# Optimization experiments

Measured on AMD Instinct MI355X. Metric: run time of the kernel, lower is better.

The kernel has to match this reference:

```python
import math
import jax, jax.numpy as jnp
import numpy as np

N_HEAD = 16

def setup_inputs() -> dict:
    key = jax.random.key(0)
    k1, k2, k3 = jax.random.split(key, 3)
    B, T, C = 4, 2048, 1024
    x = jax.random.normal(k1, (B, T, C), dtype=jnp.float32)
    Wqkv = jax.random.normal(k2, (C, 3 * C), dtype=jnp.float32) * (1.0 / math.sqrt(C))
    bqkv = jnp.zeros((3 * C,), dtype=jnp.float32)
    Wproj = jax.random.normal(k3, (C, C), dtype=jnp.float32) * (1.0 / math.sqrt(C))
    bproj = jnp.zeros((C,), dtype=jnp.float32)
    return {"x": x, "Wqkv": Wqkv, "bqkv": bqkv, "Wproj": Wproj, "bproj": bproj}

def reference(x, Wqkv, bqkv, Wproj, bproj):
    B, T, C = x.shape
    H = N_HEAD
    D = C // H
    # fused QKV projection
    qkv = x @ Wqkv + bqkv                      # [B,T,3C]
    qkv = qkv.reshape(B, T, 3, H, D).transpose(0, 2, 3, 1, 4)  # [B,3,H,T,D]
    q, k, v = qkv[:, 0], qkv[:, 1], qkv[:, 2]  # each [B,H,T,D]
    scale = 1.0 / math.sqrt(D)
    att = jnp.einsum('bhtd,bhsd->bhts', q, k) * scale  # [B,H,T,T]
    # causal mask: disallow s > t
    mask = jnp.triu(jnp.ones((T, T), dtype=bool), k=1)
    att = jnp.where(mask, jnp.float32(-1e9), att)
    att = jax.nn.softmax(att, axis=-1)
    y = jnp.einsum('bhts,bhsd->bhtd', att, v)  # [B,H,T,D]
    y = y.transpose(0, 2, 1, 3).reshape(B, T, C)
    y = y @ Wproj + bproj
    return y
```

## Files before the change

### kernel.cpp

```cpp
#include <hip/hip_runtime.h>
#include <hip/hip_bf16.h>

#define B_ 4
#define T_ 2048
#define C_ 1024
#define H_ 16
#define D_ 64

typedef __attribute__((ext_vector_type(8))) short short8;
typedef __attribute__((ext_vector_type(4))) float f32x4;

#define QSCALE 0.18033688011112042f

static __device__ __forceinline__ unsigned short f2bf(float f) {
  unsigned u = __float_as_uint(f);
  u += 0x7fff + ((u >> 16) & 1);
  return (unsigned short)(u >> 16);
}

static __device__ __forceinline__ float fast_exp2(float x) {
#if __has_builtin(__builtin_amdgcn_exp2f)
  return __builtin_amdgcn_exp2f(x);
#else
  return exp2f(x);
#endif
}

#define GL2LDS16(g, l)                                              \
  __builtin_amdgcn_global_load_lds(                                 \
      (const __attribute__((address_space(1))) void*)(g),           \
      (__attribute__((address_space(3))) void*)(l), 16, 0, 0)

__global__ __launch_bounds__(256) void convert_bf16(const float* __restrict__ in,
                                                    ushort* __restrict__ out) {
  const size_t i = ((size_t)blockIdx.x * 256 + threadIdx.x) * 4;
  float4 v = *(const float4*)(in + i);
  ushort4 o = {f2bf(v.x), f2bf(v.y), f2bf(v.z), f2bf(v.w)};
  *(ushort4*)(out + i) = o;
}

__global__ __launch_bounds__(256) void convert_transpose(
    const float* __restrict__ in, ushort* __restrict__ out, int K, int N) {
  __shared__ ushort tile[32][33];
  const int k0 = blockIdx.y << 5, n0 = blockIdx.x << 5;
  const int r = threadIdx.x >> 3;
  const int c4 = (threadIdx.x & 7) << 2;
  float4 v = *(const float4*)(in + (size_t)(k0 + r) * N + n0 + c4);
  tile[c4 + 0][r] = f2bf(v.x);
  tile[c4 + 1][r] = f2bf(v.y);
  tile[c4 + 2][r] = f2bf(v.z);
  tile[c4 + 3][r] = f2bf(v.w);
  __syncthreads();
  ushort4 o = {tile[r][c4], tile[r][c4 + 1], tile[r][c4 + 2], tile[r][c4 + 3]};
  *(ushort4*)(out + (size_t)(n0 + r) * K + k0 + c4) = o;
}

__global__ __launch_bounds__(256) void gemm_qkv_mfma(
    const ushort* __restrict__ A,
    const ushort* __restrict__ Bt,
    const float* __restrict__ bias,
    ushort* __restrict__ q, ushort* __restrict__ k, ushort* __restrict__ v) {
  __shared__ __align__(16) ushort As[128 * 32];
  __shared__ __align__(16) ushort Bs[128 * 32];
  const int tid = threadIdx.x;
  const int wave = tid >> 6, lane = tid & 63;
  const int c = lane & 15, quad = lane >> 4;
  const int wm = wave & 1, wn = wave >> 1;
  const int m0 = blockIdx.y << 7;
  const int n0 = blockIdx.x << 7;

  f32x4 acc[4][4];
#pragma unroll
  for (int i = 0; i < 4; ++i)
#pragma unroll
    for (int j = 0; j < 4; ++j) acc[i][j] = (f32x4){0.f, 0.f, 0.f, 0.f};

  for (int k0 = 0; k0 < C_; k0 += 32) {
    __syncthreads();
#pragma unroll
    for (int p = 0; p < 2; ++p) {
      const int flat = p * 4096 + wave * 1024 + lane * 16;
      const int row = flat >> 6, ke = (flat & 63) >> 1;
      GL2LDS16(A + (size_t)(m0 + row) * C_ + k0 + ke,
               (char*)As + p * 4096 + wave * 1024);
      GL2LDS16(Bt + (size_t)(n0 + row) * C_ + k0 + ke,
               (char*)Bs + p * 4096 + wave * 1024);
    }
    __syncthreads();

    short8 af[4], bf[4];
#pragma unroll
    for (int i = 0; i < 4; ++i)
      af[i] = *(const short8*)(As + (wm * 64 + i * 16 + c) * 32 + quad * 8);
#pragma unroll
    for (int j = 0; j < 4; ++j)
      bf[j] = *(const short8*)(Bs + (wn * 64 + j * 16 + c) * 32 + quad * 8);
#pragma unroll
    for (int i = 0; i < 4; ++i)
#pragma unroll
      for (int j = 0; j < 4; ++j)
        acc[i][j] =
            __builtin_amdgcn_mfma_f32_16x16x32_bf16(af[i], bf[j], acc[i][j], 0, 0, 0);
  }

  const int s = n0 >> 10;
  if (s == 2) {
#pragma unroll
    for (int j = 0; j < 4; ++j) {
      const int n = n0 + wn * 64 + j * 16 + c;
      const int h = (n >> 6) & 15, d = n & 63;
      const float bval = bias[n];
#pragma unroll
      for (int i = 0; i < 4; ++i) {
        const int m = m0 + wm * 64 + i * 16 + quad * 4;
        const int b = m >> 11, t = m & 2047;
        ushort4 pk = {f2bf(acc[i][j][0] + bval), f2bf(acc[i][j][1] + bval),
                      f2bf(acc[i][j][2] + bval), f2bf(acc[i][j][3] + bval)};
        *(ushort4*)(v + (((size_t)((b << 4) + h) << 6) + d) * T_ + t) = pk;
      }
    }
  } else {
    ushort* outp = (s == 0) ? q : k;
    const float sc = (s == 0) ? QSCALE : 1.0f;
#pragma unroll
    for (int j = 0; j < 4; ++j) {
      const int n = n0 + wn * 64 + j * 16 + c;
      const int h = (n >> 6) & 15, d = n & 63;
      const float bval = bias[n];
#pragma unroll
      for (int i = 0; i < 4; ++i) {
#pragma unroll
        for (int r = 0; r < 4; ++r) {
          const int m = m0 + wm * 64 + i * 16 + quad * 4 + r;
          const int b = m >> 11, t = m & 2047;
          outp[(((size_t)((b << 4) + h) << 11) + t) * 64 + d] =
              f2bf((acc[i][j][r] + bval) * sc);
        }
      }
    }
  }
}

__global__ __launch_bounds__(256) void gemm_proj_mfma(
    const ushort* __restrict__ A,
    const ushort* __restrict__ Bt,
    const float* __restrict__ bias,
    float* __restrict__ out) {
  __shared__ __align__(16) ushort As[128 * 32];
  __shared__ __align__(16) ushort Bs[128 * 32];
  const int tid = threadIdx.x;
  const int wave = tid >> 6, lane = tid & 63;
  const int c = lane & 15, quad = lane >> 4;
  const int wm = wave & 1, wn = wave >> 1;
  const int m0 = blockIdx.y << 7;
  const int n0 = blockIdx.x << 7;

  f32x4 acc[4][4];
#pragma unroll
  for (int i = 0; i < 4; ++i)
#pragma unroll
    for (int j = 0; j < 4; ++j) acc[i][j] = (f32x4){0.f, 0.f, 0.f, 0.f};

  for (int k0 = 0; k0 < C_; k0 += 32) {
    __syncthreads();
#pragma unroll
    for (int p = 0; p < 2; ++p) {
      const int flat = p * 4096 + wave * 1024 + lane * 16;
      const int row = flat >> 6, ke = (flat & 63) >> 1;
      GL2LDS16(A + (size_t)(m0 + row) * C_ + k0 + ke,
               (char*)As + p * 4096 + wave * 1024);
      GL2LDS16(Bt + (size_t)(n0 + row) * C_ + k0 + ke,
               (char*)Bs + p * 4096 + wave * 1024);
    }
    __syncthreads();

    short8 af[4], bf[4];
#pragma unroll
    for (int i = 0; i < 4; ++i)
      af[i] = *(const short8*)(As + (wm * 64 + i * 16 + c) * 32 + quad * 8);
#pragma unroll
    for (int j = 0; j < 4; ++j)
      bf[j] = *(const short8*)(Bs + (wn * 64 + j * 16 + c) * 32 + quad * 8);
#pragma unroll
    for (int i = 0; i < 4; ++i)
#pragma unroll
      for (int j = 0; j < 4; ++j)
        acc[i][j] =
            __builtin_amdgcn_mfma_f32_16x16x32_bf16(af[i], bf[j], acc[i][j], 0, 0, 0);
  }

#pragma unroll
  for (int j = 0; j < 4; ++j) {
    const int n = n0 + wn * 64 + j * 16 + c;
    const float bval = bias[n];
#pragma unroll
    for (int i = 0; i < 4; ++i) {
#pragma unroll
      for (int r = 0; r < 4; ++r) {
        const int m = m0 + wm * 64 + i * 16 + quad * 4 + r;
        out[(size_t)m * C_ + n] = acc[i][j][r] + bval;
      }
    }
  }
}

__global__ __launch_bounds__(256) void attn(const ushort* __restrict__ q,
                                            const ushort* __restrict__ k,
                                            const ushort* __restrict__ v,
                                            ushort* __restrict__ y2) {
  const int qt = 31 - (int)(blockIdx.x >> 6);
  const int bh = blockIdx.x & 63;
  const int t0 = qt << 6;
  const int w = threadIdx.x >> 6;
  const int lane = threadIdx.x & 63;
  const int c = lane & 15;
  const int quad = lane >> 4;

  const ushort* qp = q + (size_t)bh * T_ * D_;
  const ushort* kp = k + (size_t)bh * T_ * D_;
  const ushort* vp = v + (size_t)bh * D_ * T_;

  __shared__ __align__(16) ushort Ks[64][72];
  __shared__ __align__(16) ushort Vs[64][72];
  __shared__ __align__(16) ushort Ps[4][16][72];

  short8 qf0, qf1;
  {
    const ushort* qrow = qp + (size_t)(t0 + 16 * w + c) * D_;
    qf0 = *(const short8*)(qrow + quad * 8);
    qf1 = *(const short8*)(qrow + 32 + quad * 8);
  }

  const int srow = threadIdx.x >> 2;
  const int soff = (threadIdx.x & 3) << 4;

  uint4 ka, kb, va, vb;
  {
    const ushort* ks = kp + (size_t)srow * D_ + soff;
    const ushort* vs = vp + (size_t)srow * T_ + soff;
    ka = *(const uint4*)(ks);
    kb = *(const uint4*)(ks + 8);
    va = *(const uint4*)(vs);
    vb = *(const uint4*)(vs + 8);
  }

  f32x4 o[4];
  float l_i[4];
#pragma unroll
  for (int nt = 0; nt < 4; ++nt) o[nt] = (f32x4){0.f, 0.f, 0.f, 0.f};
#pragma unroll
  for (int r = 0; r < 4; ++r) l_i[r] = 0.f;

  for (int ib = 0; ib <= qt; ++ib) {
    __syncthreads();
    *(uint4*)(&Ks[srow][soff]) = ka;
    *(uint4*)(&Ks[srow][soff + 8]) = kb;
    *(uint4*)(&Vs[srow][soff]) = va;
    *(uint4*)(&Vs[srow][soff + 8]) = vb;
    __syncthreads();

    if (ib < qt) {
      const int s1 = (ib + 1) << 6;
      const ushort* ks = kp + (size_t)(s1 + srow) * D_ + soff;
      const ushort* vs = vp + (size_t)srow * T_ + s1 + soff;
      ka = *(const uint4*)(ks);
      kb = *(const uint4*)(ks + 8);
      va = *(const uint4*)(vs);
      vb = *(const uint4*)(vs + 8);
    }

    f32x4 s[4];
#pragma unroll
    for (int nt = 0; nt < 4; ++nt) {
      short8 kf0 = *(const short8*)(&Ks[nt * 16 + c][quad * 8]);
      short8 kf1 = *(const short8*)(&Ks[nt * 16 + c][32 + quad * 8]);
      f32x4 acc = (f32x4){0.f, 0.f, 0.f, 0.f};
      acc = __builtin_amdgcn_mfma_f32_16x16x32_bf16(qf0, kf0, acc, 0, 0, 0);
      acc = __builtin_amdgcn_mfma_f32_16x16x32_bf16(qf1, kf1, acc, 0, 0, 0);
      s[nt] = acc;
    }

    if (ib == qt) {
#pragma unroll
      for (int nt = 0; nt < 4; ++nt)
#pragma unroll
        for (int r = 0; r < 4; ++r)
          if (nt * 16 + c > 16 * w + 4 * quad + r) s[nt][r] = -1e30f;
    }

#pragma unroll
    for (int nt = 0; nt < 4; ++nt) {
#pragma unroll
      for (int r = 0; r < 4; ++r) {
        float p = fast_exp2(s[nt][r]);
        l_i[r] += p;
        Ps[w][4 * quad + r][nt * 16 + c] = f2bf(p);
      }
    }

    short8 pf0 = *(const short8*)(&Ps[w][c][quad * 8]);
    short8 pf1 = *(const short8*)(&Ps[w][c][32 + quad * 8]);
#pragma unroll
    for (int nt = 0; nt < 4; ++nt) {
      short8 vf0 = *(const short8*)(&Vs[nt * 16 + c][quad * 8]);
      short8 vf1 = *(const short8*)(&Vs[nt * 16 + c][32 + quad * 8]);
      o[nt] = __builtin_amdgcn_mfma_f32_16x16x32_bf16(pf0, vf0, o[nt], 0, 0, 0);
      o[nt] = __builtin_amdgcn_mfma_f32_16x16x32_bf16(pf1, vf1, o[nt], 0, 0, 0);
    }
  }

  float linv[4];
#pragma unroll
  for (int r = 0; r < 4; ++r) {
    float ls = l_i[r];
#pragma unroll
    for (int off = 1; off < 16; off <<= 1) ls += __shfl_xor(ls, off);
    linv[r] = 1.0f / ls;
  }

  const int b = bh >> 4, h = bh & 15;
#pragma unroll
  for (int nt = 0; nt < 4; ++nt)
#pragma unroll
    for (int r = 0; r < 4; ++r) {
      const int row = t0 + 16 * w + 4 * quad + r;
      y2[(size_t)(b * T_ + row) * C_ + h * D_ + nt * 16 + c] =
          f2bf(o[nt][r] * linv[r]);
    }
}

extern "C" void kernel_launch(void* const* d_in, const int* in_sizes, int n_in,
                              void* d_out, int out_size, void* d_ws,
                              size_t ws_size, hipStream_t stream) {
  const float* x = (const float*)d_in[0];
  const float* Wqkv = (const float*)d_in[1];
  const float* bqkv = (const float*)d_in[2];
  const float* Wproj = (const float*)d_in[3];
  const float* bproj = (const float*)d_in[4];
  float* out = (float*)d_out;

  const size_t per = (size_t)B_ * H_ * T_ * D_;
  ushort* q = (ushort*)d_ws;
  ushort* k = q + per;
  ushort* v = k + per;
  ushort* y2 = v + per;
  ushort* xb = y2 + per;
  ushort* Wqkvt = xb + per;
  ushort* Wprojt = Wqkvt + 3 * C_ * C_;

  convert_bf16<<<dim3(8192), 256, 0, stream>>>(x, xb);
  convert_transpose<<<dim3(96, 32), 256, 0, stream>>>(Wqkv, Wqkvt, C_, 3 * C_);
  convert_transpose<<<dim3(32, 32), 256, 0, stream>>>(Wproj, Wprojt, C_, C_);

  gemm_qkv_mfma<<<dim3(24, 64), 256, 0, stream>>>(xb, Wqkvt, bqkv, q, k, v);
  attn<<<dim3(2048), 256, 0, stream>>>(q, k, v, y2);
  gemm_proj_mfma<<<dim3(8, 64), 256, 0, stream>>>(y2, Wprojt, bproj, out);
}
```

Baseline: 268.1 us.

## Fuse prepass kernels, swizzle GEMM LDS layout, widen attention query tile

Merges the three conversion kernels into one launch. Applies an XOR swizzle to the GEMM LDS tiles so fragment reads avoid bank conflicts. Doubles the attention query tile to 128 rows per block, with each wave handling two 16-row groups, so each loaded K/V tile serves more queries. It also computes S^T so probabilities are written with vector stores. The trade-off is more registers in attention and half as many blocks.

```diff
diff --git a/kernel.cpp b/kernel.cpp
--- a/kernel.cpp
+++ b/kernel.cpp
@@ -31,18 +31,29 @@
       (const __attribute__((address_space(1))) void*)(g),           \
       (__attribute__((address_space(3))) void*)(l), 16, 0, 0)
 
-__global__ __launch_bounds__(256) void convert_bf16(const float* __restrict__ in,
-                                                    ushort* __restrict__ out) {
-  const size_t i = ((size_t)blockIdx.x * 256 + threadIdx.x) * 4;
-  float4 v = *(const float4*)(in + i);
-  ushort4 o = {f2bf(v.x), f2bf(v.y), f2bf(v.z), f2bf(v.w)};
-  *(ushort4*)(out + i) = o;
-}
-
-__global__ __launch_bounds__(256) void convert_transpose(
-    const float* __restrict__ in, ushort* __restrict__ out, int K, int N) {
+__global__ __launch_bounds__(256) void prepass(
+    const float* __restrict__ x, const float* __restrict__ Wq,
+    const float* __restrict__ Wp, ushort* __restrict__ xb,
+    ushort* __restrict__ Wqt, ushort* __restrict__ Wpt) {
   __shared__ ushort tile[32][33];
-  const int k0 = blockIdx.y << 5, n0 = blockIdx.x << 5;
+  const int bid = blockIdx.x;
+  if (bid < 8192) {
+    const size_t i = ((size_t)bid * 256 + threadIdx.x) * 4;
+    float4 vv = *(const float4*)(x + i);
+    ushort4 o = {f2bf(vv.x), f2bf(vv.y), f2bf(vv.z), f2bf(vv.w)};
+    *(ushort4*)(xb + i) = o;
+    return;
+  }
+  const float* in;
+  ushort* out;
+  int N, tix;
+  if (bid < 8192 + 3072) {
+    in = Wq; out = Wqt; N = 3 * C_; tix = bid - 8192;
+  } else {
+    in = Wp; out = Wpt; N = C_; tix = bid - 11264;
+  }
+  const int nT = N >> 5;
+  const int k0 = (tix / nT) << 5, n0 = (tix % nT) << 5;
   const int r = threadIdx.x >> 3;
   const int c4 = (threadIdx.x & 7) << 2;
   float4 v = *(const float4*)(in + (size_t)(k0 + r) * N + n0 + c4);
@@ -52,14 +63,27 @@
   tile[c4 + 3][r] = f2bf(v.w);
   __syncthreads();
   ushort4 o = {tile[r][c4], tile[r][c4 + 1], tile[r][c4 + 2], tile[r][c4 + 3]};
-  *(ushort4*)(out + (size_t)(n0 + r) * K + k0 + c4) = o;
+  *(ushort4*)(out + (size_t)(n0 + r) * C_ + k0 + c4) = o;
+}
+
+static __device__ __forceinline__ void swz_src(int wave, int lane, int p,
+                                               int& row, int& off) {
+  const int f = p * 256 + wave * 64 + lane;
+  const int P = f >> 3, pos = f & 7;
+  const int x = pos ^ (P & 7);
+  row = 2 * P + (x >> 2);
+  off = (x & 3) * 8;
+}
+static __device__ __forceinline__ int swz_frag(int r, int quad) {
+  const int P = r >> 1;
+  const int pos = (((r & 1) << 2) | quad) ^ (P & 7);
+  return (P * 8 + pos) * 16;
 }
 
 __global__ __launch_bounds__(256) void gemm_qkv_mfma(
-    const ushort* __restrict__ A,
-    const ushort* __restrict__ Bt,
-    const float* __restrict__ bias,
-    ushort* __restrict__ q, ushort* __restrict__ k, ushort* __restrict__ v) {
+    const ushort* __restrict__ A, const ushort* __restrict__ Bt,
+    const float* __restrict__ bias, ushort* __restrict__ q,
+    ushort* __restrict__ k, ushort* __restrict__ v) {
   __shared__ __align__(16) ushort As[128 * 32];
   __shared__ __align__(16) ushort Bs[128 * 32];
   const int tid = threadIdx.x;
@@ -69,6 +93,15 @@
   const int m0 = blockIdx.y << 7;
   const int n0 = blockIdx.x << 7;
 
+  int srcRow[2], srcOff[2];
+#pragma unroll
+  for (int p = 0; p < 2; ++p) swz_src(wave, lane, p, srcRow[p], srcOff[p]);
+  int fOffA[4], fOffB[4];
+#pragma unroll
+  for (int i = 0; i < 4; ++i) fOffA[i] = swz_frag(wm * 64 + i * 16 + c, quad);
+#pragma unroll
+  for (int j = 0; j < 4; ++j) fOffB[j] = swz_frag(wn * 64 + j * 16 + c, quad);
+
   f32x4 acc[4][4];
 #pragma unroll
   for (int i = 0; i < 4; ++i)
@@ -79,11 +112,9 @@
     __syncthreads();
 #pragma unroll
     for (int p = 0; p < 2; ++p) {
-      const int flat = p * 4096 + wave * 1024 + lane * 16;
-      const int row = flat >> 6, ke = (flat & 63) >> 1;
-      GL2LDS16(A + (size_t)(m0 + row) * C_ + k0 + ke,
+      GL2LDS16(A + (size_t)(m0 + srcRow[p]) * C_ + k0 + srcOff[p],
                (char*)As + p * 4096 + wave * 1024);
-      GL2LDS16(Bt + (size_t)(n0 + row) * C_ + k0 + ke,
+      GL2LDS16(Bt + (size_t)(n0 + srcRow[p]) * C_ + k0 + srcOff[p],
                (char*)Bs + p * 4096 + wave * 1024);
     }
     __syncthreads();
@@ -91,10 +122,10 @@
     short8 af[4], bf[4];
 #pragma unroll
     for (int i = 0; i < 4; ++i)
-      af[i] = *(const short8*)(As + (wm * 64 + i * 16 + c) * 32 + quad * 8);
+      af[i] = *(const short8*)((const char*)As + fOffA[i]);
 #pragma unroll
     for (int j = 0; j < 4; ++j)
-      bf[j] = *(const short8*)(Bs + (wn * 64 + j * 16 + c) * 32 + quad * 8);
+      bf[j] = *(const short8*)((const char*)Bs + fOffB[j]);
 #pragma unroll
     for (int i = 0; i < 4; ++i)
 #pragma unroll
@@ -142,10 +173,8 @@
 }
 
 __global__ __launch_bounds__(256) void gemm_proj_mfma(
-    const ushort* __restrict__ A,
-    const ushort* __restrict__ Bt,
-    const float* __restrict__ bias,
-    float* __restrict__ out) {
+    const ushort* __restrict__ A, const ushort* __restrict__ Bt,
+    const float* __restrict__ bias, float* __restrict__ out) {
   __shared__ __align__(16) ushort As[128 * 32];
   __shared__ __align__(16) ushort Bs[128 * 32];
   const int tid = threadIdx.x;
@@ -155,6 +184,15 @@
   const int m0 = blockIdx.y << 7;
   const int n0 = blockIdx.x << 7;
 
+  int srcRow[2], srcOff[2];
+#pragma unroll
+  for (int p = 0; p < 2; ++p) swz_src(wave, lane, p, srcRow[p], srcOff[p]);
+  int fOffA[4], fOffB[4];
+#pragma unroll
+  for (int i = 0; i < 4; ++i) fOffA[i] = swz_frag(wm * 64 + i * 16 + c, quad);
+#pragma unroll
+  for (int j = 0; j < 4; ++j) fOffB[j] = swz_frag(wn * 64 + j * 16 + c, quad);
+
   f32x4 acc[4][4];
 #pragma unroll
   for (int i = 0; i < 4; ++i)
@@ -165,11 +203,9 @@
     __syncthreads();
 #pragma unroll
     for (int p = 0; p < 2; ++p) {
-      const int flat = p * 4096 + wave * 1024 + lane * 16;
-      const int row = flat >> 6, ke = (flat & 63) >> 1;
-      GL2LDS16(A + (size_t)(m0 + row) * C_ + k0 + ke,
+      GL2LDS16(A + (size_t)(m0 + srcRow[p]) * C_ + k0 + srcOff[p],
                (char*)As + p * 4096 + wave * 1024);
-      GL2LDS16(Bt + (size_t)(n0 + row) * C_ + k0 + ke,
+      GL2LDS16(Bt + (size_t)(n0 + srcRow[p]) * C_ + k0 + srcOff[p],
                (char*)Bs + p * 4096 + wave * 1024);
     }
     __syncthreads();
@@ -177,10 +213,10 @@
     short8 af[4], bf[4];
 #pragma unroll
     for (int i = 0; i < 4; ++i)
-      af[i] = *(const short8*)(As + (wm * 64 + i * 16 + c) * 32 + quad * 8);
+      af[i] = *(const short8*)((const char*)As + fOffA[i]);
 #pragma unroll
     for (int j = 0; j < 4; ++j)
-      bf[j] = *(const short8*)(Bs + (wn * 64 + j * 16 + c) * 32 + quad * 8);
+      bf[j] = *(const short8*)((const char*)Bs + fOffB[j]);
 #pragma unroll
     for (int i = 0; i < 4; ++i)
 #pragma unroll
@@ -208,9 +244,9 @@
                                             const ushort* __restrict__ k,
                                             const ushort* __restrict__ v,
                                             ushort* __restrict__ y2) {
-  const int qt = 31 - (int)(blockIdx.x >> 6);
+  const int qt = 15 - (int)(blockIdx.x >> 6);
   const int bh = blockIdx.x & 63;
-  const int t0 = qt << 6;
+  const int t0 = qt << 7;
   const int w = threadIdx.x >> 6;
   const int lane = threadIdx.x & 63;
   const int c = lane & 15;
@@ -222,13 +258,14 @@
 
   __shared__ __align__(16) ushort Ks[64][72];
   __shared__ __align__(16) ushort Vs[64][72];
-  __shared__ __align__(16) ushort Ps[4][16][72];
-
-  short8 qf0, qf1;
-  {
-    const ushort* qrow = qp + (size_t)(t0 + 16 * w + c) * D_;
-    qf0 = *(const short8*)(qrow + quad * 8);
-    qf1 = *(const short8*)(qrow + 32 + quad * 8);
+  __shared__ __align__(16) ushort Ps[4][32][72];
+
+  short8 qf[2][2];
+#pragma unroll
+  for (int g = 0; g < 2; ++g) {
+    const ushort* qrow = qp + (size_t)(t0 + 32 * w + 16 * g + c) * D_;
+    qf[g][0] = *(const short8*)(qrow + quad * 8);
+    qf[g][1] = *(const short8*)(qrow + 32 + quad * 8);
   }
 
   const int srow = threadIdx.x >> 2;
@@ -244,14 +281,16 @@
     vb = *(const uint4*)(vs + 8);
   }
 
-  f32x4 o[4];
-  float l_i[4];
-#pragma unroll
-  for (int nt = 0; nt < 4; ++nt) o[nt] = (f32x4){0.f, 0.f, 0.f, 0.f};
-#pragma unroll
-  for (int r = 0; r < 4; ++r) l_i[r] = 0.f;
-
-  for (int ib = 0; ib <= qt; ++ib) {
+  f32x4 o[2][4];
+  float l_i[2] = {0.f, 0.f};
+#pragma unroll
+  for (int g = 0; g < 2; ++g)
+#pragma unroll
+    for (int dt = 0; dt < 4; ++dt) o[g][dt] = (f32x4){0.f, 0.f, 0.f, 0.f};
+
+  const int nb = 2 * qt + 2;
+  for (int ib = 0; ib < nb; ++ib) {
+    const int s0 = ib << 6;
     __syncthreads();
     *(uint4*)(&Ks[srow][soff]) = ka;
     *(uint4*)(&Ks[srow][soff + 8]) = kb;
@@ -259,7 +298,7 @@
     *(uint4*)(&Vs[srow][soff + 8]) = vb;
     __syncthreads();
 
-    if (ib < qt) {
+    if (ib + 1 < nb) {
       const int s1 = (ib + 1) << 6;
       const ushort* ks = kp + (size_t)(s1 + srow) * D_ + soff;
       const ushort* vs = vp + (size_t)srow * T_ + s1 + soff;
@@ -269,64 +308,83 @@
       vb = *(const uint4*)(vs + 8);
     }
 
-    f32x4 s[4];
-#pragma unroll
-    for (int nt = 0; nt < 4; ++nt) {
-      short8 kf0 = *(const short8*)(&Ks[nt * 16 + c][quad * 8]);
-      short8 kf1 = *(const short8*)(&Ks[nt * 16 + c][32 + quad * 8]);
-      f32x4 acc = (f32x4){0.f, 0.f, 0.f, 0.f};
-      acc = __builtin_amdgcn_mfma_f32_16x16x32_bf16(qf0, kf0, acc, 0, 0, 0);
-      acc = __builtin_amdgcn_mfma_f32_16x16x32_bf16(qf1, kf1, acc, 0, 0, 0);
-      s[nt] = acc;
-    }
-
-    if (ib == qt) {
-#pragma unroll
-      for (int nt = 0; nt < 4; ++nt)
-#pragma unroll
-        for (int r = 0; r < 4; ++r)
-          if (nt * 16 + c > 16 * w + 4 * quad + r) s[nt][r] = -1e30f;
-    }
-
-#pragma unroll
-    for (int nt = 0; nt < 4; ++nt) {
-#pragma unroll
-      for (int r = 0; r < 4; ++r) {
-        float p = fast_exp2(s[nt][r]);
-        l_i[r] += p;
-        Ps[w][4 * quad + r][nt * 16 + c] = f2bf(p);
-      }
-    }
-
-    short8 pf0 = *(const short8*)(&Ps[w][c][quad * 8]);
-    short8 pf1 = *(const short8*)(&Ps[w][c][32 + quad * 8]);
-#pragma unroll
-    for (int nt = 0; nt < 4; ++nt) {
-      short8 vf0 = *(const short8*)(&Vs[nt * 16 + c][quad * 8]);
-      short8 vf1 = *(const short8*)(&Vs[nt * 16 + c][32 + quad * 8]);
-      o[nt] = __builtin_amdgcn_mfma_f32_16x16x32_bf16(pf0, vf0, o[nt], 0, 0, 0);
-      o[nt] = __builtin_amdgcn_mfma_f32_16x16x32_bf16(pf1, vf1, o[nt], 0, 0, 0);
-    }
-  }
-
-  float linv[4];
-#pragma unroll
-  for (int r = 0; r < 4; ++r) {
-    float ls = l_i[r];
-#pragma unroll
-    for (int off = 1; off < 16; off <<= 1) ls += __shfl_xor(ls, off);
-    linv[r] = 1.0f / ls;
+#pragma unroll
+    for (int g = 0; g < 2; ++g) {
+      f32x4 st[4];
+#pragma unroll
+      for (int kt = 0; kt < 4; ++kt) {
+        short8 af0 = *(const short8*)(&Ks[kt * 16 + c][quad * 8]);
+        short8 af1 = *(const short8*)(&Ks[kt * 16 + c][32 + quad * 8]);
+        f32x4 a = (f32x4){0.f, 0.f, 0.f, 0.f};
+        a = __builtin_amdgcn_mfma_f32_16x16x32_bf16(af0, qf[g][0], a, 0, 0, 0);
+        a = __builtin_amdgcn_mfma_f32_16x16x32_bf16(af1, qf[g][1], a, 0, 0, 0);
+        st[kt] = a;
+      }
+
+      const int qbase = t0 + 32 * w + 16 * g;
+      if (s0 + 63 > qbase) {
+#pragma unroll
+        for (int kt = 0; kt < 4; ++kt)
+#pragma unroll
+          for (int r = 0; r < 4; ++r)
+            if (s0 + kt * 16 + 4 * quad + r > qbase + c) st[kt][r] = -1e30f;
+      }
+
+      float lacc = 0.f;
+#pragma unroll
+      for (int kt = 0; kt < 4; ++kt) {
+        float p0 = fast_exp2(st[kt][0]);
+        float p1 = fast_exp2(st[kt][1]);
+        float p2 = fast_exp2(st[kt][2]);
+        float p3 = fast_exp2(st[kt][3]);
+        lacc += (p0 + p1) + (p2 + p3);
+        ushort4 pk = {f2bf(p0), f2bf(p1), f2bf(p2), f2bf(p3)};
+        *(ushort4*)(&Ps[w][g * 16 + c][kt * 16 + 4 * quad]) = pk;
+      }
+      l_i[g] += lacc;
+    }
+
+    short8 pf[2][2];
+#pragma unroll
+    for (int g = 0; g < 2; ++g) {
+      pf[g][0] = *(const short8*)(&Ps[w][g * 16 + c][quad * 8]);
+      pf[g][1] = *(const short8*)(&Ps[w][g * 16 + c][32 + quad * 8]);
+    }
+#pragma unroll
+    for (int dt = 0; dt < 4; ++dt) {
+      short8 vf0 = *(const short8*)(&Vs[dt * 16 + c][quad * 8]);
+      short8 vf1 = *(const short8*)(&Vs[dt * 16 + c][32 + quad * 8]);
+#pragma unroll
+      for (int g = 0; g < 2; ++g) {
+        o[g][dt] =
+            __builtin_amdgcn_mfma_f32_16x16x32_bf16(vf0, pf[g][0], o[g][dt], 0, 0, 0);
+        o[g][dt] =
+            __builtin_amdgcn_mfma_f32_16x16x32_bf16(vf1, pf[g][1], o[g][dt], 0, 0, 0);
+      }
+    }
+  }
+
+  float linv[2];
+#pragma unroll
+  for (int g = 0; g < 2; ++g) {
+    float ls = l_i[g];
+    ls += __shfl_xor(ls, 16);
+    ls += __shfl_xor(ls, 32);
+    linv[g] = 1.0f / ls;
   }
 
   const int b = bh >> 4, h = bh & 15;
 #pragma unroll
-  for (int nt = 0; nt < 4; ++nt)
-#pragma unroll
-    for (int r = 0; r < 4; ++r) {
-      const int row = t0 + 16 * w + 4 * quad + r;
-      y2[(size_t)(b * T_ + row) * C_ + h * D_ + nt * 16 + c] =
-          f2bf(o[nt][r] * linv[r]);
-    }
+  for (int g = 0; g < 2; ++g) {
+    const int row = t0 + 32 * w + 16 * g + c;
+    ushort* dst = y2 + (size_t)(b * T_ + row) * C_ + h * 64;
+#pragma unroll
+    for (int dt = 0; dt < 4; ++dt) {
+      ushort4 ov = {f2bf(o[g][dt][0] * linv[g]), f2bf(o[g][dt][1] * linv[g]),
+                    f2bf(o[g][dt][2] * linv[g]), f2bf(o[g][dt][3] * linv[g])};
+      *(ushort4*)(dst + dt * 16 + 4 * quad) = ov;
+    }
+  }
 }
 
 extern "C" void kernel_launch(void* const* d_in, const int* in_sizes, int n_in,
@@ -348,11 +406,8 @@
   ushort* Wqkvt = xb + per;
   ushort* Wprojt = Wqkvt + 3 * C_ * C_;
 
-  convert_bf16<<<dim3(8192), 256, 0, stream>>>(x, xb);
-  convert_transpose<<<dim3(96, 32), 256, 0, stream>>>(Wqkv, Wqkvt, C_, 3 * C_);
-  convert_transpose<<<dim3(32, 32), 256, 0, stream>>>(Wproj, Wprojt, C_, C_);
-
+  prepass<<<dim3(12288), 256, 0, stream>>>(x, Wqkv, Wproj, xb, Wqkvt, Wprojt);
   gemm_qkv_mfma<<<dim3(24, 64), 256, 0, stream>>>(xb, Wqkvt, bqkv, q, k, v);
-  attn<<<dim3(2048), 256, 0, stream>>>(q, k, v, y2);
+  attn<<<dim3(1024), 256, 0, stream>>>(q, k, v, y2);
   gemm_proj_mfma<<<dim3(8, 64), 256, 0, stream>>>(y2, Wprojt, bproj, out);
 }
```

New measurement: 261.7 us. 2.4% less time.
